# Kernel optimization log

Hardware: AMD Instinct MI355X
Metric: run time of the kernel (lower is better)

Reference implementation:

```python
import jax, jax.numpy as jnp
import numpy as np
from jax import lax

B, T_ENC, T_DEC, H = 512, 64, 18, 128
NF = 17  # input_size - 1 (column 14 is dropped)
COLS = np.array(list(range(14)) + list(range(15, 18)))


def _lstm_cell(x, h, c, Wih, Whh, bih, bhh):
    # PyTorch LSTMCell: gates = x@Wih^T + bih + h@Whh^T + bhh, order i,f,g,o
    g = x @ Wih.T + bih + h @ Whh.T + bhh
    i, f, gg, o = jnp.split(g, 4, axis=-1)
    c2 = jax.nn.sigmoid(f) * c + jax.nn.sigmoid(i) * jnp.tanh(gg)
    h2 = jax.nn.sigmoid(o) * jnp.tanh(c2)
    return h2, c2


def setup_inputs() -> dict:
    key = jax.random.key(0)
    ks = jax.random.split(key, 32)
    s = 0.08
    def w(k, shape):
        return jax.random.normal(k, shape, jnp.float32) * s
    return {
        "input_p_q": jax.random.normal(ks[0], (B, T_ENC, 18), jnp.float32),
        "label_p": jax.random.normal(ks[1], (B, T_ENC), jnp.float32),
        "Wih1": w(ks[2], (4 * H, NF)), "Whh1": w(ks[3], (4 * H, H)),
        "bih1": w(ks[4], (4 * H,)), "bhh1": w(ks[5], (4 * H,)),
        "Wih2": w(ks[6], (4 * H, H + 1)), "Whh2": w(ks[7], (4 * H, H)),
        "bih2": w(ks[8], (4 * H,)), "bhh2": w(ks[9], (4 * H,)),
        "Wihd": w(ks[10], (4 * H, H)), "Whhd": w(ks[11], (4 * H, H)),
        "bihd": w(ks[12], (4 * H,)), "bhhd": w(ks[13], (4 * H,)),
        "Wi_w": w(ks[14], (T_ENC, T_ENC)), "Wi_b": w(ks[15], (T_ENC,)),
        "We_w": w(ks[16], (T_ENC, 2 * H)),
        "Vd_w": w(ks[17], (1, T_ENC)), "Vd_b": w(ks[18], (1,)),
        "Wi2_w": w(ks[19], (T_ENC, T_ENC)), "Wi2_b": w(ks[20], (T_ENC,)),
        "We2_w": w(ks[21], (T_ENC, 2 * H)),
        "Vd2_w": w(ks[22], (1, T_ENC)), "Vd2_b": w(ks[23], (1,)),
        "Wx_w": w(ks[24], (H, H)), "Wx_b": w(ks[25], (H,)),
        "Wh_w": w(ks[26], (H, 2 * H)),
        "V_w": w(ks[27], (1, H)), "V_b": w(ks[28], (1,)),
        "reg_w": w(ks[29], (1, H)), "reg_b": w(ks[30], (1,)),
    }


def reference(input_p_q, label_p, Wih1, Whh1, bih1, bhh1, Wih2, Whh2, bih2, bhh2,
              Wihd, Whhd, bihd, bhhd, Wi_w, Wi_b, We_w, Vd_w, Vd_b,
              Wi2_w, Wi2_b, We2_w, Vd2_w, Vd2_b, Wx_w, Wx_b, Wh_w, V_w, V_b,
              reg_w, reg_b):
    B_ = input_p_q.shape[0]
    inputs = input_p_q[:, :T_ENC, COLS]  # [B, T, 17]
    z = jnp.zeros((B_, H), input_p_q.dtype)

    # stage 1: per-step spatial attention over the 17 driving series + LSTM encoder
    WiX = jnp.swapaxes(inputs, 1, 2) @ Wi_w.T + Wi_b  # [B, 17, T] (step-invariant)
    def step1(carry, x_t):
        h, c = carry
        e = jnp.concatenate([h, c], axis=-1) @ We_w.T  # [B, T]
        score = jnp.tanh(WiX + e[:, None, :]) @ Vd_w[0] + Vd_b[0]  # [B, 17]
        a = jax.nn.softmax(score, axis=1)
        h, c = _lstm_cell(x_t * a, h, c, Wih1, Whh1, bih1, bhh1)
        return (h, c), h
    _, mid = lax.scan(step1, (z, z), jnp.swapaxes(inputs, 0, 1))
    mid = jnp.swapaxes(mid, 0, 1)  # [B, T, H]
    mid2 = jnp.concatenate([mid, label_p[:, :T_ENC, None]], axis=2)  # [B, T, H+1]

    # stage 2: spatial attention over H+1 channels + second LSTM encoder
    Wi2X = jnp.swapaxes(mid2, 1, 2) @ Wi2_w.T + Wi2_b  # [B, H+1, T]
    def step2(carry, x_t):
        h, c = carry
        e = jnp.concatenate([h, c], axis=-1) @ We2_w.T  # [B, T]
        score = jnp.tanh(Wi2X + e[:, None, :]) @ Vd2_w[0] + Vd2_b[0]  # [B, H+1]
        a = jax.nn.softmax(score, axis=1)
        h, c = _lstm_cell(x_t * a, h, c, Wih2, Whh2, bih2, bhh2)
        return (h, c), h
    _, final = lax.scan(step2, (z, z), jnp.swapaxes(mid2, 0, 1))
    final = jnp.swapaxes(final, 0, 1)  # [B, T, H]

    # stage 3: temporal attention decoder for T_DEC + 6 steps
    WxF = final @ Wx_w.T + Wx_b  # [B, T, H] (step-invariant)
    def step3(carry, _):
        h, c = carry
        e = jnp.concatenate([h, c], axis=-1) @ Wh_w.T  # [B, H]
        s = jnp.tanh(WxF + e[:, None, :]) @ V_w[0] + V_b[0]  # [B, T]
        a = jax.nn.softmax(s, axis=1)
        din = jnp.einsum('bt,bth->bh', a, final)  # context vector
        h, c = _lstm_cell(din, h, c, Wihd, Whhd, bihd, bhhd)
        return (h, c), h
    _, dec = lax.scan(step3, (z, z), None, length=T_DEC + 6)
    dec = jnp.swapaxes(dec, 0, 1)  # [B, T_DEC+6, H]
    out = dec @ reg_w[0] + reg_b[0]  # [B, T_DEC+6]
    return out[:, -T_DEC:]
```

## Files before the change

kernel.cpp:

```cpp
#include <hip/hip_runtime.h>
#include <hip/hip_fp16.h>

#define TENC 64
#define TDEC 18
#define NDEC 24
#define NF1  17
#define NF2  129
#define HH   128

#define OFF_WI   0
#define OFF_WI2  4096
#define U_GB   8192
#define U_GDH  45568
#define U_GDX  78336
#define U_GFH  111616
#define U_GFX  144384
#define U_WE   177152
#define U_WE2  185344
#define U_WH   193536
#define U_WXH  209920

#define SB   68
#define SWF  132
#define XIN  1200
#define BIGN 8772

typedef _Float16 h2t __attribute__((ext_vector_type(2)));

#if defined(__has_builtin)
#if __has_builtin(__builtin_amdgcn_fdot2)
#define HAVE_FDOT2 1
#endif
#endif

template<int I> struct ic_t { static constexpr int v = I; };
template<int N, typename F>
__device__ __forceinline__ void sfor(F&& f)
{
    if constexpr (N > 0) { sfor<N - 1>((F&&)f); f(ic_t<N - 1>{}); }
}

__device__ __forceinline__ float fdot2p(unsigned w, unsigned x, float acc)
{
    h2t hw = __builtin_bit_cast(h2t, w);
    h2t hx = __builtin_bit_cast(h2t, x);
#ifdef HAVE_FDOT2
    return __builtin_amdgcn_fdot2(hw, hx, acc, false);
#else
    return acc + (float)hw.x * (float)hx.x + (float)hw.y * (float)hx.y;
#endif
}

__device__ __forceinline__ unsigned pkh_d(float a, float b)
{
    __half ha = __float2half(a), hb = __float2half(b);
    return (unsigned)__half_as_ushort(ha) | ((unsigned)__half_as_ushort(hb) << 16);
}

__device__ __forceinline__ float hget(unsigned u, int hi)
{
    h2t v = __builtin_bit_cast(h2t, u);
    return hi ? (float)v.y : (float)v.x;
}

__device__ __forceinline__ float fsig(float x) { return 1.f / (1.f + __expf(-x)); }
__device__ __forceinline__ float ftanh(float x)
{
    x = fminf(fmaxf(x, -15.f), 15.f);
    float e = __expf(2.f * x);
    return (e - 1.f) / (e + 1.f);
}

__global__ void pack_f2(const float* Wi, const float* Wi2, float* ws)
{
    const int m = blockIdx.y;
    const float* src = m ? Wi2 : Wi;
    const int off = m ? OFF_WI2 : OFF_WI;
    const int G = 64, K = 64, n = G * K;
    for (int i = blockIdx.x * blockDim.x + threadIdx.x; i < n; i += gridDim.x * blockDim.x) {
        int q = i & 3, gk = i >> 2;
        int kk = gk / G, g = gk - kk * G;
        ws[off + i] = src[g * K + kk * 4 + q];
    }
}

__global__ void pack_gp(const float* Wih, const float* Whh, int Kx, int KXP, int qbase,
                        unsigned base, int ldg, unsigned* wsu)
{
    const int g = threadIdx.x;
    const int q = qbase + blockIdx.x;
    int k0 = 2 * q, k1 = 2 * q + 1;
    float f0 = (k0 < KXP) ? ((k0 < Kx) ? Wih[g * Kx + k0] : 0.f) : Whh[g * HH + (k0 - KXP)];
    float f1 = (k1 < KXP) ? ((k1 < Kx) ? Wih[g * Kx + k1] : 0.f) : Whh[g * HH + (k1 - KXP)];
    wsu[base + (unsigned)blockIdx.x * (unsigned)ldg + g] = pkh_d(f0, f1);
}

__global__ void pack_ew(const float* W, int J, int nPQ, int nI, unsigned base, unsigned* wsu)
{
    int idx = blockIdx.x * blockDim.x + threadIdx.x;
    if (idx >= J * 128) return;
    int j = idx >> 7, r = idx & 127;
    int pq = r / nI, i = r - pq * nI;
    int pr = i * nPQ + pq;
    wsu[base + idx] = pkh_d(W[j * 256 + 2 * pr], W[j * 256 + 2 * pr + 1]);
}

__global__ __launch_bounds__(512, 2)
void dstp_main(const float* __restrict__ inq, const float* __restrict__ labp,
               const float* __restrict__ bih1, const float* __restrict__ bhh1,
               const float* __restrict__ bih2, const float* __restrict__ bhh2,
               const float* __restrict__ bihd, const float* __restrict__ bhhd,
               const float* __restrict__ Wi_b, const float* __restrict__ Vd_w, const float* __restrict__ Vd_b,
               const float* __restrict__ Wi2_b, const float* __restrict__ Vd2_w, const float* __restrict__ Vd2_b,
               const float* __restrict__ Wx_b, const float* __restrict__ V_w, const float* __restrict__ V_b,
               const float* __restrict__ reg_w, const float* __restrict__ reg_b,
               const float* __restrict__ ws, float* __restrict__ out)
{
    __shared__ __align__(16) unsigned buf_h[2][TENC][64];
    __shared__ __align__(16) float big[2][BIGN];
    __shared__ __align__(16) unsigned hcp[2][128];
    __shared__ __align__(16) unsigned xhp[2][132];
    __shared__ __align__(16) float ebuf[2][128];
    __shared__ float sc[2][132];
    __shared__ float att[2][64];
    __shared__ float pre[2][512];
    __shared__ float preH[2][512];
    __shared__ float lab[2][64];
    __shared__ __align__(16) float vw1[64], vw2[64], vwf[128], rw[128];
    __shared__ float rsm[4];

    const int tid  = threadIdx.x;
    const int b0   = blockIdx.x * 2;
    const unsigned* wsu = (const unsigned*)ws;
    const float4* Wip  = (const float4*)(ws + OFF_WI);
    const float4* Wi2p = (const float4*)(ws + OFF_WI2);

    const float bg1 = bih1[tid] + bhh1[tid];
    const float bg2 = bih2[tid] + bhh2[tid];
    const float bgd = bihd[tid] + bhhd[tid];
    float creg = 0.f;

    if (tid < 128) lab[tid >> 6][tid & 63] = labp[(b0 + (tid >> 6)) * TENC + (tid & 63)];
    if (tid < 64)        vw1[tid]       = Vd_w[tid];
    else if (tid < 128)  vw2[tid - 64]  = Vd2_w[tid - 64];
    else if (tid < 256)  vwf[tid - 128] = V_w[tid - 128];
    else if (tid < 384)  rw[tid - 256]  = reg_w[tid - 256];
    for (int i = tid; i < 2176; i += 512) {
        int bb = i / 1088, r = i - bb * 1088, t = r / NF1, f = r - t * NF1;
        big[bb][XIN + r] = inq[((b0 + bb) * TENC + t) * 18 + f + (f >= 14)];
    }
    __syncthreads();
    for (int i = tid; i < 2176; i += 512) {
        int bb = i / 1088, r = i - bb * 1088, f = r >> 6, j = r & 63;
        float acc = Wi_b[j];
        for (int tt = 0; tt < 16; ++tt) {
            float4 w = Wip[tt * 64 + j];
            acc += big[bb][XIN + (4 * tt + 0) * NF1 + f] * w.x
                 + big[bb][XIN + (4 * tt + 1) * NF1 + f] * w.y
                 + big[bb][XIN + (4 * tt + 2) * NF1 + f] * w.z
                 + big[bb][XIN + (4 * tt + 3) * NF1 + f] * w.w;
        }
        big[bb][f * SB + j] = acc;
    }

    {
        if (tid < 256) hcp[tid >> 7][tid & 127] = 0u;
        if (tid < 264) xhp[tid / 132][tid % 132] = 0u;
        creg = 0.f;
        unsigned wB[73];
        sfor<73>([&](auto I) { wB[I.v] = wsu[U_GB + I.v * 512 + tid]; });
        unsigned we[16];
        const int ewb = U_WE + ((tid >> 3) << 7) + ((tid & 7) << 4);
        sfor<16>([&](auto I) { we[I.v] = wsu[ewb + I.v]; });
        __syncthreads();

        for (int t = 0; t < TENC; ++t) {
            {
                int j = tid >> 3, pq = tid & 7;
                float a0 = 0.f, a1 = 0.f, b0c = 0.f, b1c = 0.f;
                sfor<8>([&](auto I) {
                    a0  = fdot2p(we[I.v], hcp[0][I.v * 8 + pq], a0);
                    a1  = fdot2p(we[I.v], hcp[1][I.v * 8 + pq], a1);
                    b0c = fdot2p(we[8 + I.v], hcp[0][(8 + I.v) * 8 + pq], b0c);
                    b1c = fdot2p(we[8 + I.v], hcp[1][(8 + I.v) * 8 + pq], b1c);
                });
                float s0 = a0 + b0c, s1 = a1 + b1c;
                s0 += __shfl_xor(s0, 1, 8); s1 += __shfl_xor(s1, 1, 8);
                s0 += __shfl_xor(s0, 2, 8); s1 += __shfl_xor(s1, 2, 8);
                s0 += __shfl_xor(s0, 4, 8); s1 += __shfl_xor(s1, 4, 8);
                if (pq == 0) { ebuf[0][j] = s0; ebuf[1][j] = s1; }
            }
            __syncthreads();
            {
                const uint4* h0q = (const uint4*)hcp[0];
                const uint4* h1q = (const uint4*)hcp[1];
                float q0 = 0.f, q1 = 0.f, q2 = 0.f, q3 = 0.f;
                sfor<16>([&](auto C) {
                    uint4 H0 = h0q[C.v], H1 = h1q[C.v];
                    q0 = fdot2p(wB[9 + 4 * C.v + 0], H0.x, q0);
                    q2 = fdot2p(wB[9 + 4 * C.v + 0], H1.x, q2);
                    q1 = fdot2p(wB[9 + 4 * C.v + 1], H0.y, q1);
                    q3 = fdot2p(wB[9 + 4 * C.v + 1], H1.y, q3);
                    q0 = fdot2p(wB[9 + 4 * C.v + 2], H0.z, q0);
                    q2 = fdot2p(wB[9 + 4 * C.v + 2], H1.z, q2);
                    q1 = fdot2p(wB[9 + 4 * C.v + 3], H0.w, q1);
                    q3 = fdot2p(wB[9 + 4 * C.v + 3], H1.w, q3);
                });
                preH[0][tid] = q0 + q1;
                preH[1][tid] = q2 + q3;
            }
            for (int i = tid; i < 544; i += 512) {
                int bb = i / 272, r = i - bb * 272, f = r >> 4, pp = r & 15;
                float4 wx = *(const float4*)&big[bb][f * SB + pp * 4];
                float4 e4 = *(const float4*)&ebuf[bb][pp * 4];
                float4 v4 = *(const float4*)&vw1[pp * 4];
                float acc = ftanh(wx.x + e4.x) * v4.x + ftanh(wx.y + e4.y) * v4.y
                          + ftanh(wx.z + e4.z) * v4.z + ftanh(wx.w + e4.w) * v4.w;
                acc += __shfl_xor(acc, 1, 16);
                acc += __shfl_xor(acc, 2, 16);
                acc += __shfl_xor(acc, 4, 16);
                acc += __shfl_xor(acc, 8, 16);
                if (pp == 0) sc[bb][f] = acc + Vd_b[0];
            }
            __syncthreads();
            if (tid < 128) {
                int bb = tid >> 6, l = tid & 63;
                float e = (l < NF1) ? __expf(sc[bb][l]) : 0.f;
                float s = e;
                for (int d = 32; d; d >>= 1) s += __shfl_xor(s, d, 64);
                float xv = (l < NF1) ? big[bb][XIN + t * NF1 + l] * (e / s) : 0.f;
                float xp = __shfl_xor(xv, 1, 64);
                if (!(l & 1) && l < 18) xhp[bb][l >> 1] = pkh_d(xv, xp);
            }
            __syncthreads();
            {
                const uint4* x0q = (const uint4*)xhp[0];
                const uint4* x1q = (const uint4*)xhp[1];
                float p00 = bg1, p10 = bg1;
                sfor<2>([&](auto C) {
                    uint4 X0 = x0q[C.v], X1 = x1q[C.v];
                    p00 = fdot2p(wB[4 * C.v + 0], X0.x, p00);
                    p10 = fdot2p(wB[4 * C.v + 0], X1.x, p10);
                    p00 = fdot2p(wB[4 * C.v + 1], X0.y, p00);
                    p10 = fdot2p(wB[4 * C.v + 1], X1.y, p10);
                    p00 = fdot2p(wB[4 * C.v + 2], X0.z, p00);
                    p10 = fdot2p(wB[4 * C.v + 2], X1.z, p10);
                    p00 = fdot2p(wB[4 * C.v + 3], X0.w, p00);
                    p10 = fdot2p(wB[4 * C.v + 3], X1.w, p10);
                });
                p00 = fdot2p(wB[8], xhp[0][8], p00);
                p10 = fdot2p(wB[8], xhp[1][8], p10);
                pre[0][tid] = p00 + preH[0][tid];
                pre[1][tid] = p10 + preH[1][tid];
            }
            __syncthreads();
            if (tid < 256) {
                int bb = tid >> 7, k = tid & 127;
                float gi = pre[bb][k], gf = pre[bb][128 + k], gg = pre[bb][256 + k], go = pre[bb][384 + k];
                float c2 = fsig(gf) * creg + fsig(gi) * ftanh(gg);
                float h2v = fsig(go) * ftanh(c2);
                creg = c2;
                float hp = __shfl_xor(h2v, 1, 64);
                float cp = __shfl_xor(c2, 1, 64);
                if (!(k & 1)) {
                    unsigned hu = pkh_d(h2v, hp);
                    hcp[bb][k >> 1] = hu;
                    hcp[bb][64 + (k >> 1)] = pkh_d(c2, cp);
                    buf_h[bb][t][k >> 1] = hu;
                }
            }
            __syncthreads();
        }
    }

    if (tid < 256) hcp[tid >> 7][tid & 127] = 0u;
    if (tid < 264) xhp[tid / 132][tid % 132] = 0u;
    creg = 0.f;
    for (int i = tid; i < 16512; i += 512) {
        int bb = i / 8256, r = i - bb * 8256, f = r >> 6, j = r & 63;
        float acc = Wi2_b[j];
        if (f < HH) {
            int fp = f >> 1, fh = f & 1;
            for (int tt = 0; tt < 16; ++tt) {
                float4 w = Wi2p[tt * 64 + j];
                acc += hget(buf_h[bb][4 * tt + 0][fp], fh) * w.x
                     + hget(buf_h[bb][4 * tt + 1][fp], fh) * w.y
                     + hget(buf_h[bb][4 * tt + 2][fp], fh) * w.z
                     + hget(buf_h[bb][4 * tt + 3][fp], fh) * w.w;
            }
        } else {
            for (int tt = 0; tt < 16; ++tt) {
                float4 w = Wi2p[tt * 64 + j];
                acc += lab[bb][4 * tt] * w.x + lab[bb][4 * tt + 1] * w.y
                     + lab[bb][4 * tt + 2] * w.z + lab[bb][4 * tt + 3] * w.w;
            }
        }
        big[bb][f * SB + j] = acc;
    }

    {
        unsigned wD[129];
        sfor<65>([&](auto I) { wD[I.v] = wsu[U_GDX + I.v * 512 + tid]; });
        sfor<64>([&](auto I) { wD[65 + I.v] = wsu[U_GDH + I.v * 512 + tid]; });
        unsigned wes[16];
        const int ewb2 = U_WE2 + ((tid >> 3) << 7) + ((tid & 7) << 4);
        sfor<16>([&](auto I) { wes[I.v] = wsu[ewb2 + I.v]; });
        __syncthreads();

        for (int t = 0; t < TENC; ++t) {
            {
                int j = tid >> 3, pq = tid & 7;
                float a0 = 0.f, a1 = 0.f, b0c = 0.f, b1c = 0.f;
                sfor<8>([&](auto I) {
                    a0  = fdot2p(wes[I.v], hcp[0][I.v * 8 + pq], a0);
                    a1  = fdot2p(wes[I.v], hcp[1][I.v * 8 + pq], a1);
                    b0c = fdot2p(wes[8 + I.v], hcp[0][(8 + I.v) * 8 + pq], b0c);
                    b1c = fdot2p(wes[8 + I.v], hcp[1][(8 + I.v) * 8 + pq], b1c);
                });
                float s0 = a0 + b0c, s1 = a1 + b1c;
                s0 += __shfl_xor(s0, 1, 8); s1 += __shfl_xor(s1, 1, 8);
                s0 += __shfl_xor(s0, 2, 8); s1 += __shfl_xor(s1, 2, 8);
                s0 += __shfl_xor(s0, 4, 8); s1 += __shfl_xor(s1, 4, 8);
                if (pq == 0) { ebuf[0][j] = s0; ebuf[1][j] = s1; }
            }
            __syncthreads();
            {
                const uint4* h0q = (const uint4*)hcp[0];
                const uint4* h1q = (const uint4*)hcp[1];
                float q0 = 0.f, q1 = 0.f, q2 = 0.f, q3 = 0.f;
                sfor<16>([&](auto C) {
                    uint4 H0 = h0q[C.v], H1 = h1q[C.v];
                    q0 = fdot2p(wD[65 + 4 * C.v + 0], H0.x, q0);
                    q2 = fdot2p(wD[65 + 4 * C.v + 0], H1.x, q2);
                    q1 = fdot2p(wD[65 + 4 * C.v + 1], H0.y, q1);
                    q3 = fdot2p(wD[65 + 4 * C.v + 1], H1.y, q3);
                    q0 = fdot2p(wD[65 + 4 * C.v + 2], H0.z, q0);
                    q2 = fdot2p(wD[65 + 4 * C.v + 2], H1.z, q2);
                    q1 = fdot2p(wD[65 + 4 * C.v + 3], H0.w, q1);
                    q3 = fdot2p(wD[65 + 4 * C.v + 3], H1.w, q3);
                });
                preH[0][tid] = q0 + q1;
                preH[1][tid] = q2 + q3;
            }
            for (int i = tid; i < 1032; i += 512) {
                int bb = i / 516, r = i - bb * 516, f = r >> 2, pp = r & 3;
                float acc = 0.f;
                #pragma unroll
                for (int c = 0; c < 4; ++c) {
                    float4 wx = *(const float4*)&big[bb][f * SB + pp * 16 + c * 4];
                    float4 e4 = *(const float4*)&ebuf[bb][pp * 16 + c * 4];
                    float4 v4 = *(const float4*)&vw2[pp * 16 + c * 4];
                    acc += ftanh(wx.x + e4.x) * v4.x + ftanh(wx.y + e4.y) * v4.y
                         + ftanh(wx.z + e4.z) * v4.z + ftanh(wx.w + e4.w) * v4.w;
                }
                acc += __shfl_xor(acc, 1, 4);
                acc += __shfl_xor(acc, 2, 4);
                if (pp == 0) sc[bb][f] = acc + Vd2_b[0];
            }
            __syncthreads();
            if (tid < 128) {
                int bb = tid >> 6, l = tid & 63;
                float e1 = __expf(sc[bb][l]);
                float e2 = __expf(sc[bb][l + 64]);
                float e3 = (l == 0) ? __expf(sc[bb][128]) : 0.f;
                float s = e1 + e2 + e3;
                for (int d = 32; d; d >>= 1) s += __shfl_xor(s, d, 64);
                float inv = 1.f / s;
                float v1 = hget(buf_h[bb][t][l >> 1], l & 1) * e1 * inv;
                float v2 = hget(buf_h[bb][t][32 + (l >> 1)], l & 1) * e2 * inv;
                float v1p = __shfl_xor(v1, 1, 64);
                float v2p = __shfl_xor(v2, 1, 64);
                if (!(l & 1)) {
                    xhp[bb][l >> 1] = pkh_d(v1, v1p);
                    xhp[bb][32 + (l >> 1)] = pkh_d(v2, v2p);
                }
                if (l == 0) xhp[bb][64] = pkh_d(lab[bb][t] * e3 * inv, 0.f);
            }
            __syncthreads();
            {
                const uint4* x0q = (const uint4*)xhp[0];
                const uint4* x1q = (const uint4*)xhp[1];
                float p00 = bg2, p01 = 0.f, p10 = bg2, p11 = 0.f;
                sfor<16>([&](auto C) {
                    uint4 X0 = x0q[C.v], X1 = x1q[C.v];
                    p00 = fdot2p(wD[4 * C.v + 0], X0.x, p00);
                    p10 = fdot2p(wD[4 * C.v + 0], X1.x, p10);
                    p01 = fdot2p(wD[4 * C.v + 1], X0.y, p01);
                    p11 = fdot2p(wD[4 * C.v + 1], X1.y, p11);
                    p00 = fdot2p(wD[4 * C.v + 2], X0.z, p00);
                    p10 = fdot2p(wD[4 * C.v + 2], X1.z, p10);
                    p01 = fdot2p(wD[4 * C.v + 3], X0.w, p01);
                    p11 = fdot2p(wD[4 * C.v + 3], X1.w, p11);
                });
                p00 = fdot2p(wD[64], xhp[0][64], p00);
                p10 = fdot2p(wD[64], xhp[1][64], p10);
                pre[0][tid] = (p00 + p01) + preH[0][tid];
                pre[1][tid] = (p10 + p11) + preH[1][tid];
            }
            __syncthreads();
            if (tid < 256) {
                int bb = tid >> 7, k = tid & 127;
                float gi = pre[bb][k], gf = pre[bb][128 + k], gg = pre[bb][256 + k], go = pre[bb][384 + k];
                float c2 = fsig(gf) * creg + fsig(gi) * ftanh(gg);
                float h2v = fsig(go) * ftanh(c2);
                creg = c2;
                float hp = __shfl_xor(h2v, 1, 64);
                float cp = __shfl_xor(c2, 1, 64);
                if (!(k & 1)) {
                    unsigned hu = pkh_d(h2v, hp);
                    hcp[bb][k >> 1] = hu;
                    hcp[bb][64 + (k >> 1)] = pkh_d(c2, cp);
                    buf_h[bb][t][k >> 1] = hu;
                }
            }
            __syncthreads();
        }
    }

    if (tid < 256) hcp[tid >> 7][tid & 127] = 0u;
    if (tid < 264) xhp[tid / 132][tid % 132] = 0u;
    creg = 0.f;
    {
        const int j = tid & 127;
        unsigned wxh[64];
        sfor<64>([&](auto I) { wxh[I.v] = wsu[U_WXH + I.v * 128 + j]; });
        for (int u = tid >> 7; u < 128; u += 4) {
            int bb = u >> 6, tt = u & 63;
            const uint4* bq = (const uint4*)buf_h[bb][tt];
            float a0 = Wx_b[j], a1 = 0.f, a2 = 0.f, a3 = 0.f;
            sfor<16>([&](auto C) {
                uint4 X = bq[C.v];
                a0 = fdot2p(wxh[4 * C.v + 0], X.x, a0);
                a1 = fdot2p(wxh[4 * C.v + 1], X.y, a1);
                a2 = fdot2p(wxh[4 * C.v + 2], X.z, a2);
                a3 = fdot2p(wxh[4 * C.v + 3], X.w, a3);
            });
            big[bb][tt * SWF + j] = (a0 + a1) + (a2 + a3);
        }
    }

    {
        unsigned wF[128];
        sfor<64>([&](auto I) { wF[I.v] = wsu[U_GFX + I.v * 512 + tid]; });
        sfor<64>([&](auto I) { wF[64 + I.v] = wsu[U_GFH + I.v * 512 + tid]; });
        unsigned wh[32];
        const int whb = U_WH + ((tid >> 2) << 7) + ((tid & 3) << 5);
        sfor<32>([&](auto I) { wh[I.v] = wsu[whb + I.v]; });
        __syncthreads();

        for (int n = 0; n < NDEC; ++n) {
            {
                int j = tid >> 2, pq = tid & 3;
                float a0 = 0.f, a1 = 0.f, b0c = 0.f, b1c = 0.f;
                sfor<16>([&](auto I) {
                    a0  = fdot2p(wh[I.v], hcp[0][I.v * 4 + pq], a0);
                    a1  = fdot2p(wh[I.v], hcp[1][I.v * 4 + pq], a1);
                    b0c = fdot2p(wh[16 + I.v], hcp[0][(16 + I.v) * 4 + pq], b0c);
                    b1c = fdot2p(wh[16 + I.v], hcp[1][(16 + I.v) * 4 + pq], b1c);
                });
                float s0 = a0 + b0c, s1 = a1 + b1c;
                s0 += __shfl_xor(s0, 1, 4); s1 += __shfl_xor(s1, 1, 4);
                s0 += __shfl_xor(s0, 2, 4); s1 += __shfl_xor(s1, 2, 4);
                if (pq == 0) { ebuf[0][j] = s0; ebuf[1][j] = s1; }
            }
            __syncthreads();
            {
                const uint4* h0q = (const uint4*)hcp[0];
                const uint4* h1q = (const uint4*)hcp[1];
                float q0 = 0.f, q1 = 0.f, q2 = 0.f, q3 = 0.f;
                sfor<16>([&](auto C) {
                    uint4 H0 = h0q[C.v], H1 = h1q[C.v];
                    q0 = fdot2p(wF[64 + 4 * C.v + 0], H0.x, q0);
                    q2 = fdot2p(wF[64 + 4 * C.v + 0], H1.x, q2);
                    q1 = fdot2p(wF[64 + 4 * C.v + 1], H0.y, q1);
                    q3 = fdot2p(wF[64 + 4 * C.v + 1], H1.y, q3);
                    q0 = fdot2p(wF[64 + 4 * C.v + 2], H0.z, q0);
                    q2 = fdot2p(wF[64 + 4 * C.v + 2], H1.z, q2);
                    q1 = fdot2p(wF[64 + 4 * C.v + 3], H0.w, q1);
                    q3 = fdot2p(wF[64 + 4 * C.v + 3], H1.w, q3);
                });
                preH[0][tid] = q0 + q1;
                preH[1][tid] = q2 + q3;
            }
            for (int i = tid; i < 1024; i += 512) {
                int bb = i >> 9, r = i & 511, tt = r >> 3, pp = r & 7;
                float acc = 0.f;
                #pragma unroll
                for (int c = 0; c < 4; ++c) {
                    float4 wx = *(const float4*)&big[bb][tt * SWF + pp * 16 + c * 4];
                    float4 e4 = *(const float4*)&ebuf[bb][pp * 16 + c * 4];
                    float4 v4 = *(const float4*)&vwf[pp * 16 + c * 4];
                    acc += ftanh(wx.x + e4.x) * v4.x + ftanh(wx.y + e4.y) * v4.y
                         + ftanh(wx.z + e4.z) * v4.z + ftanh(wx.w + e4.w) * v4.w;
                }
                acc += __shfl_xor(acc, 1, 8);
                acc += __shfl_xor(acc, 2, 8);
                acc += __shfl_xor(acc, 4, 8);
                if (pp == 0) sc[bb][tt] = acc + V_b[0];
            }
            __syncthreads();
            if (tid < 128) {
                int bb = tid >> 6, l = tid & 63;
                float e = __expf(sc[bb][l]);
                float s = e;
                for (int d = 32; d; d >>= 1) s += __shfl_xor(s, d, 64);
                att[bb][l] = e / s;
            }
            __syncthreads();
            for (int i = tid; i < 1024; i += 512) {
                int bb = i >> 9, r = i & 511, k = r >> 2, pq = r & 3;
                int kp = k >> 1, kh = k & 1;
                float acc = 0.f;
                #pragma unroll
                for (int u = 0; u < 16; ++u) {
                    int tt = u * 4 + pq;
                    acc += att[bb][tt] * hget(buf_h[bb][tt][kp], kh);
                }
                acc += __shfl_xor(acc, 1, 64);
                acc += __shfl_xor(acc, 2, 64);
                float dp = __shfl_xor(acc, 4, 64);
                if ((r & 7) == 0) xhp[bb][r >> 3] = pkh_d(acc, dp);
            }
            __syncthreads();
            {
                const uint4* x0q = (const uint4*)xhp[0];
                const uint4* x1q = (const uint4*)xhp[1];
                float p00 = bgd, p01 = 0.f, p10 = bgd, p11 = 0.f;
                sfor<16>([&](auto C) {
                    uint4 X0 = x0q[C.v], X1 = x1q[C.v];
                    p00 = fdot2p(wF[4 * C.v + 0], X0.x, p00);
                    p10 = fdot2p(wF[4 * C.v + 0], X1.x, p10);
                    p01 = fdot2p(wF[4 * C.v + 1], X0.y, p01);
                    p11 = fdot2p(wF[4 * C.v + 1], X1.y, p11);
                    p00 = fdot2p(wF[4 * C.v + 2], X0.z, p00);
                    p10 = fdot2p(wF[4 * C.v + 2], X1.z, p10);
                    p01 = fdot2p(wF[4 * C.v + 3], X0.w, p01);
                    p11 = fdot2p(wF[4 * C.v + 3], X1.w, p11);
                });
                pre[0][tid] = (p00 + p01) + preH[0][tid];
                pre[1][tid] = (p10 + p11) + preH[1][tid];
            }
            __syncthreads();
            if (tid < 256) {
                int bb = tid >> 7, k = tid & 127;
                float gi = pre[bb][k], gf = pre[bb][128 + k], gg = pre[bb][256 + k], go = pre[bb][384 + k];
                float c2 = fsig(gf) * creg + fsig(gi) * ftanh(gg);
                float h2v = fsig(go) * ftanh(c2);
                creg = c2;
                float hp = __shfl_xor(h2v, 1, 64);
                float cp = __shfl_xor(c2, 1, 64);
                if (!(k & 1)) {
                    unsigned hu = pkh_d(h2v, hp);
                    hcp[bb][k >> 1] = hu;
                    hcp[bb][64 + (k >> 1)] = pkh_d(c2, cp);
                }
                if (n >= 6) {
                    float v = h2v * rw[k];
                    for (int d = 32; d; d >>= 1) v += __shfl_xor(v, d, 64);
                    if ((tid & 63) == 0) rsm[tid >> 6] = v;
                }
            }
            __syncthreads();
            if (n >= 6 && tid < 2)
                out[(b0 + tid) * TDEC + (n - 6)] = rsm[tid * 2] + rsm[tid * 2 + 1] + reg_b[0];
        }
    }
}

extern "C" void kernel_launch(void* const* d_in, const int* in_sizes, int n_in,
                              void* d_out, int out_size, void* d_ws, size_t ws_size,
                              hipStream_t stream)
{
    const float* inq   = (const float*)d_in[0];
    const float* labp  = (const float*)d_in[1];
    const float* Wih1  = (const float*)d_in[2];
    const float* Whh1  = (const float*)d_in[3];
    const float* bih1  = (const float*)d_in[4];
    const float* bhh1  = (const float*)d_in[5];
    const float* Wih2  = (const float*)d_in[6];
    const float* Whh2  = (const float*)d_in[7];
    const float* bih2  = (const float*)d_in[8];
    const float* bhh2  = (const float*)d_in[9];
    const float* Wihd  = (const float*)d_in[10];
    const float* Whhd  = (const float*)d_in[11];
    const float* bihd  = (const float*)d_in[12];
    const float* bhhd  = (const float*)d_in[13];
    const float* Wi_w  = (const float*)d_in[14];
    const float* Wi_b  = (const float*)d_in[15];
    const float* We_w  = (const float*)d_in[16];
    const float* Vd_w  = (const float*)d_in[17];
    const float* Vd_b  = (const float*)d_in[18];
    const float* Wi2_w = (const float*)d_in[19];
    const float* Wi2_b = (const float*)d_in[20];
    const float* We2_w = (const float*)d_in[21];
    const float* Vd2_w = (const float*)d_in[22];
    const float* Vd2_b = (const float*)d_in[23];
    const float* Wx_w  = (const float*)d_in[24];
    const float* Wx_b  = (const float*)d_in[25];
    const float* Wh_w  = (const float*)d_in[26];
    const float* V_w   = (const float*)d_in[27];
    const float* V_b   = (const float*)d_in[28];
    const float* reg_w = (const float*)d_in[29];
    const float* reg_b = (const float*)d_in[30];
    float* ws  = (float*)d_ws;
    unsigned* wsu = (unsigned*)d_ws;
    float* out = (float*)d_out;

    pack_f2<<<dim3(16, 2), 256, 0, stream>>>(Wi_w, Wi2_w, ws);
    pack_gp<<<73, 512, 0, stream>>>(Wih1, Whh1, 17, 18, 0, U_GB, 512, wsu);
    pack_gp<<<65, 512, 0, stream>>>(Wih2, Whh2, 129, 130, 0, U_GDX, 512, wsu);
    pack_gp<<<64, 512, 0, stream>>>(Wih2, Whh2, 129, 130, 65, U_GDH, 512, wsu);
    pack_gp<<<64, 512, 0, stream>>>(Wihd, Whhd, 128, 128, 0, U_GFX, 512, wsu);
    pack_gp<<<64, 512, 0, stream>>>(Wihd, Whhd, 128, 128, 64, U_GFH, 512, wsu);
    pack_gp<<<64, 128, 0, stream>>>(Wx_w, Wx_w, 128, 128, 0, U_WXH, 128, wsu);
    pack_ew<<<8, 1024, 0, stream>>>(We_w, 64, 8, 16, U_WE, wsu);
    pack_ew<<<8, 1024, 0, stream>>>(We2_w, 64, 8, 16, U_WE2, wsu);
    pack_ew<<<16, 1024, 0, stream>>>(Wh_w, 128, 4, 32, U_WH, wsu);
    dstp_main<<<256, 512, 0, stream>>>(inq, labp, bih1, bhh1, bih2, bhh2, bihd, bhhd,
                                       Wi_b, Vd_w, Vd_b, Wi2_b, Vd2_w, Vd2_b,
                                       Wx_b, V_w, V_b, reg_w, reg_b, ws, out);
}
```

Before: 798.9 us.

## Fuse attention score, exp and weighting into one phase with deferred softmax normalization

In all three recurrent stages, the score computation, the exponentiation and the input weighting are merged into a single phase. The softmax denominator is computed through per-wave partial sums in shared memory and applied after the gate matvec (or after the context reduction), not before. This removes one or two block-wide barriers per timestep, on a latency-bound serial recurrence. In exchange, unnormalized exp-weighted inputs are packed to half precision, which risks overflow or precision loss. Lanes with padded feature indices now do some redundant work.

```diff
diff --git a/kernel.cpp b/kernel.cpp
--- a/kernel.cpp
+++ b/kernel.cpp
@@ -121,8 +121,8 @@
     __shared__ __align__(16) unsigned hcp[2][128];
     __shared__ __align__(16) unsigned xhp[2][132];
     __shared__ __align__(16) float ebuf[2][128];
-    __shared__ float sc[2][132];
     __shared__ float att[2][64];
+    __shared__ float ssum[8][2];
     __shared__ float pre[2][512];
     __shared__ float preH[2][512];
     __shared__ float lab[2][64];
@@ -208,35 +208,58 @@
                 });
                 preH[0][tid] = q0 + q1;
                 preH[1][tid] = q2 + q3;
-            }
-            for (int i = tid; i < 544; i += 512) {
-                int bb = i / 272, r = i - bb * 272, f = r >> 4, pp = r & 15;
-                float4 wx = *(const float4*)&big[bb][f * SB + pp * 4];
-                float4 e4 = *(const float4*)&ebuf[bb][pp * 4];
-                float4 v4 = *(const float4*)&vw1[pp * 4];
-                float acc = ftanh(wx.x + e4.x) * v4.x + ftanh(wx.y + e4.y) * v4.y
-                          + ftanh(wx.z + e4.z) * v4.z + ftanh(wx.w + e4.w) * v4.w;
-                acc += __shfl_xor(acc, 1, 16);
-                acc += __shfl_xor(acc, 2, 16);
-                acc += __shfl_xor(acc, 4, 16);
-                acc += __shfl_xor(acc, 8, 16);
-                if (pp == 0) sc[bb][f] = acc + Vd_b[0];
-            }
-            __syncthreads();
-            if (tid < 128) {
-                int bb = tid >> 6, l = tid & 63;
-                float e = (l < NF1) ? __expf(sc[bb][l]) : 0.f;
-                float s = e;
-                for (int d = 32; d; d >>= 1) s += __shfl_xor(s, d, 64);
-                float xv = (l < NF1) ? big[bb][XIN + t * NF1 + l] * (e / s) : 0.f;
-                float xp = __shfl_xor(xv, 1, 64);
-                if (!(l & 1) && l < 18) xhp[bb][l >> 1] = pkh_d(xv, xp);
-            }
-            __syncthreads();
-            {
+
+                float ew0 = 0.f, ew1 = 0.f;
+                {
+                    int i = tid, bb = i / 288, r = i - bb * 288, f = r >> 4, pp = r & 15;
+                    int fc = (f < NF1) ? f : 16;
+                    float4 wx = *(const float4*)&big[bb][fc * SB + pp * 4];
+                    float4 e4 = *(const float4*)&ebuf[bb][pp * 4];
+                    float4 v4 = *(const float4*)&vw1[pp * 4];
+                    float acc = ftanh(wx.x + e4.x) * v4.x + ftanh(wx.y + e4.y) * v4.y
+                              + ftanh(wx.z + e4.z) * v4.z + ftanh(wx.w + e4.w) * v4.w;
+                    acc += __shfl_xor(acc, 1, 16);
+                    acc += __shfl_xor(acc, 2, 16);
+                    acc += __shfl_xor(acc, 4, 16);
+                    acc += __shfl_xor(acc, 8, 16);
+                    float e = (pp == 0 && f < NF1) ? __expf(acc + Vd_b[0]) : 0.f;
+                    float xval = (f < NF1) ? big[bb][XIN + t * NF1 + fc] : 0.f;
+                    float prod = xval * e;
+                    float podd = __shfl_xor(prod, 16, 64);
+                    if ((r & 31) == 0) xhp[bb][f >> 1] = pkh_d(prod, podd);
+                    ew0 += (bb == 0) ? e : 0.f;
+                    ew1 += (bb == 1) ? e : 0.f;
+                }
+                if (tid < 64) {
+                    int i = 512 + tid, bb = 1, r = i - 288, f = r >> 4, pp = r & 15;
+                    int fc = (f < NF1) ? f : 16;
+                    float4 wx = *(const float4*)&big[bb][fc * SB + pp * 4];
+                    float4 e4 = *(const float4*)&ebuf[bb][pp * 4];
+                    float4 v4 = *(const float4*)&vw1[pp * 4];
+                    float acc = ftanh(wx.x + e4.x) * v4.x + ftanh(wx.y + e4.y) * v4.y
+                              + ftanh(wx.z + e4.z) * v4.z + ftanh(wx.w + e4.w) * v4.w;
+                    acc += __shfl_xor(acc, 1, 16);
+                    acc += __shfl_xor(acc, 2, 16);
+                    acc += __shfl_xor(acc, 4, 16);
+                    acc += __shfl_xor(acc, 8, 16);
+                    float e = (pp == 0 && f < NF1) ? __expf(acc + Vd_b[0]) : 0.f;
+                    float xval = (f < NF1) ? big[bb][XIN + t * NF1 + fc] : 0.f;
+                    float prod = xval * e;
+                    float podd = __shfl_xor(prod, 16, 64);
+                    if ((r & 31) == 0) xhp[bb][f >> 1] = pkh_d(prod, podd);
+                    ew1 += e;
+                }
+                for (int d = 32; d; d >>= 1) { ew0 += __shfl_xor(ew0, d, 64); ew1 += __shfl_xor(ew1, d, 64); }
+                if ((tid & 63) == 0) { ssum[tid >> 6][0] = ew0; ssum[tid >> 6][1] = ew1; }
+            }
+            __syncthreads();
+            {
+                float S0 = 0.f, S1 = 0.f;
+                sfor<8>([&](auto W) { S0 += ssum[W.v][0]; S1 += ssum[W.v][1]; });
+                float inv0 = 1.f / S0, inv1 = 1.f / S1;
                 const uint4* x0q = (const uint4*)xhp[0];
                 const uint4* x1q = (const uint4*)xhp[1];
-                float p00 = bg1, p10 = bg1;
+                float p00 = 0.f, p10 = 0.f;
                 sfor<2>([&](auto C) {
                     uint4 X0 = x0q[C.v], X1 = x1q[C.v];
                     p00 = fdot2p(wB[4 * C.v + 0], X0.x, p00);
@@ -250,8 +273,8 @@
                 });
                 p00 = fdot2p(wB[8], xhp[0][8], p00);
                 p10 = fdot2p(wB[8], xhp[1][8], p10);
-                pre[0][tid] = p00 + preH[0][tid];
-                pre[1][tid] = p10 + preH[1][tid];
+                pre[0][tid] = p00 * inv0 + bg1 + preH[0][tid];
+                pre[1][tid] = p10 * inv1 + bg1 + preH[1][tid];
             }
             __syncthreads();
             if (tid < 256) {
@@ -341,46 +364,65 @@
                 });
                 preH[0][tid] = q0 + q1;
                 preH[1][tid] = q2 + q3;
-            }
-            for (int i = tid; i < 1032; i += 512) {
-                int bb = i / 516, r = i - bb * 516, f = r >> 2, pp = r & 3;
-                float acc = 0.f;
+
+                float ew0 = 0.f, ew1 = 0.f;
                 #pragma unroll
-                for (int c = 0; c < 4; ++c) {
-                    float4 wx = *(const float4*)&big[bb][f * SB + pp * 16 + c * 4];
-                    float4 e4 = *(const float4*)&ebuf[bb][pp * 16 + c * 4];
-                    float4 v4 = *(const float4*)&vw2[pp * 16 + c * 4];
-                    acc += ftanh(wx.x + e4.x) * v4.x + ftanh(wx.y + e4.y) * v4.y
-                         + ftanh(wx.z + e4.z) * v4.z + ftanh(wx.w + e4.w) * v4.w;
-                }
-                acc += __shfl_xor(acc, 1, 4);
-                acc += __shfl_xor(acc, 2, 4);
-                if (pp == 0) sc[bb][f] = acc + Vd2_b[0];
-            }
-            __syncthreads();
-            if (tid < 128) {
-                int bb = tid >> 6, l = tid & 63;
-                float e1 = __expf(sc[bb][l]);
-                float e2 = __expf(sc[bb][l + 64]);
-                float e3 = (l == 0) ? __expf(sc[bb][128]) : 0.f;
-                float s = e1 + e2 + e3;
-                for (int d = 32; d; d >>= 1) s += __shfl_xor(s, d, 64);
-                float inv = 1.f / s;
-                float v1 = hget(buf_h[bb][t][l >> 1], l & 1) * e1 * inv;
-                float v2 = hget(buf_h[bb][t][32 + (l >> 1)], l & 1) * e2 * inv;
-                float v1p = __shfl_xor(v1, 1, 64);
-                float v2p = __shfl_xor(v2, 1, 64);
-                if (!(l & 1)) {
-                    xhp[bb][l >> 1] = pkh_d(v1, v1p);
-                    xhp[bb][32 + (l >> 1)] = pkh_d(v2, v2p);
-                }
-                if (l == 0) xhp[bb][64] = pkh_d(lab[bb][t] * e3 * inv, 0.f);
-            }
-            __syncthreads();
-            {
+                for (int it = 0; it < 2; ++it) {
+                    int i = tid + it * 512;
+                    int bb = i / 520, r = i - bb * 520, f = r >> 2, pp = r & 3;
+                    int fc = (f < NF2) ? f : 128;
+                    float acc = 0.f;
+                    #pragma unroll
+                    for (int c = 0; c < 4; ++c) {
+                        float4 wx = *(const float4*)&big[bb][fc * SB + pp * 16 + c * 4];
+                        float4 e4 = *(const float4*)&ebuf[bb][pp * 16 + c * 4];
+                        float4 v4 = *(const float4*)&vw2[pp * 16 + c * 4];
+                        acc += ftanh(wx.x + e4.x) * v4.x + ftanh(wx.y + e4.y) * v4.y
+                             + ftanh(wx.z + e4.z) * v4.z + ftanh(wx.w + e4.w) * v4.w;
+                    }
+                    acc += __shfl_xor(acc, 1, 4);
+                    acc += __shfl_xor(acc, 2, 4);
+                    float e = (pp == 0 && f < NF2) ? __expf(acc + Vd2_b[0]) : 0.f;
+                    float xval = (f < HH) ? hget(buf_h[bb][t][fc >> 1], f & 1) : lab[bb][t];
+                    float prod = xval * e;
+                    float podd = __shfl_xor(prod, 4, 64);
+                    if ((r & 7) == 0) xhp[bb][f >> 1] = pkh_d(prod, podd);
+                    ew0 += (bb == 0) ? e : 0.f;
+                    ew1 += (bb == 1) ? e : 0.f;
+                }
+                if (tid < 16) {
+                    int i = 1024 + tid;
+                    int bb = 1, r = i - 520, f = r >> 2, pp = r & 3;
+                    int fc = (f < NF2) ? f : 128;
+                    float acc = 0.f;
+                    #pragma unroll
+                    for (int c = 0; c < 4; ++c) {
+                        float4 wx = *(const float4*)&big[bb][fc * SB + pp * 16 + c * 4];
+                        float4 e4 = *(const float4*)&ebuf[bb][pp * 16 + c * 4];
+                        float4 v4 = *(const float4*)&vw2[pp * 16 + c * 4];
+                        acc += ftanh(wx.x + e4.x) * v4.x + ftanh(wx.y + e4.y) * v4.y
+                             + ftanh(wx.z + e4.z) * v4.z + ftanh(wx.w + e4.w) * v4.w;
+                    }
+                    acc += __shfl_xor(acc, 1, 4);
+                    acc += __shfl_xor(acc, 2, 4);
+                    float e = (pp == 0 && f < NF2) ? __expf(acc + Vd2_b[0]) : 0.f;
+                    float xval = (f < HH) ? hget(buf_h[bb][t][fc >> 1], f & 1) : lab[bb][t];
+                    float prod = xval * e;
+                    float podd = __shfl_xor(prod, 4, 64);
+                    if ((r & 7) == 0) xhp[bb][f >> 1] = pkh_d(prod, podd);
+                    ew1 += e;
+                }
+                for (int d = 32; d; d >>= 1) { ew0 += __shfl_xor(ew0, d, 64); ew1 += __shfl_xor(ew1, d, 64); }
+                if ((tid & 63) == 0) { ssum[tid >> 6][0] = ew0; ssum[tid >> 6][1] = ew1; }
+            }
+            __syncthreads();
+            {
+                float S0 = 0.f, S1 = 0.f;
+                sfor<8>([&](auto W) { S0 += ssum[W.v][0]; S1 += ssum[W.v][1]; });
+                float inv0 = 1.f / S0, inv1 = 1.f / S1;
                 const uint4* x0q = (const uint4*)xhp[0];
                 const uint4* x1q = (const uint4*)xhp[1];
-                float p00 = bg2, p01 = 0.f, p10 = bg2, p11 = 0.f;
+                float p00 = 0.f, p01 = 0.f, p10 = 0.f, p11 = 0.f;
                 sfor<16>([&](auto C) {
                     uint4 X0 = x0q[C.v], X1 = x1q[C.v];
                     p00 = fdot2p(wD[4 * C.v + 0], X0.x, p00);
@@ -394,8 +436,8 @@
                 });
                 p00 = fdot2p(wD[64], xhp[0][64], p00);
                 p10 = fdot2p(wD[64], xhp[1][64], p10);
-                pre[0][tid] = (p00 + p01) + preH[0][tid];
-                pre[1][tid] = (p10 + p11) + preH[1][tid];
+                pre[0][tid] = (p00 + p01) * inv0 + bg2 + preH[0][tid];
+                pre[1][tid] = (p10 + p11) * inv1 + bg2 + preH[1][tid];
             }
             __syncthreads();
             if (tid < 256) {
@@ -481,45 +523,50 @@
                 });
                 preH[0][tid] = q0 + q1;
                 preH[1][tid] = q2 + q3;
-            }
-            for (int i = tid; i < 1024; i += 512) {
-                int bb = i >> 9, r = i & 511, tt = r >> 3, pp = r & 7;
-                float acc = 0.f;
+
+                float ew0 = 0.f, ew1 = 0.f;
                 #pragma unroll
-                for (int c = 0; c < 4; ++c) {
-                    float4 wx = *(const float4*)&big[bb][tt * SWF + pp * 16 + c * 4];
-                    float4 e4 = *(const float4*)&ebuf[bb][pp * 16 + c * 4];
-                    float4 v4 = *(const float4*)&vwf[pp * 16 + c * 4];
-                    acc += ftanh(wx.x + e4.x) * v4.x + ftanh(wx.y + e4.y) * v4.y
-                         + ftanh(wx.z + e4.z) * v4.z + ftanh(wx.w + e4.w) * v4.w;
-                }
-                acc += __shfl_xor(acc, 1, 8);
-                acc += __shfl_xor(acc, 2, 8);
-                acc += __shfl_xor(acc, 4, 8);
-                if (pp == 0) sc[bb][tt] = acc + V_b[0];
-            }
-            __syncthreads();
-            if (tid < 128) {
-                int bb = tid >> 6, l = tid & 63;
-                float e = __expf(sc[bb][l]);
-                float s = e;
-                for (int d = 32; d; d >>= 1) s += __shfl_xor(s, d, 64);
-                att[bb][l] = e / s;
-            }
-            __syncthreads();
-            for (int i = tid; i < 1024; i += 512) {
-                int bb = i >> 9, r = i & 511, k = r >> 2, pq = r & 3;
-                int kp = k >> 1, kh = k & 1;
-                float acc = 0.f;
-                #pragma unroll
-                for (int u = 0; u < 16; ++u) {
-                    int tt = u * 4 + pq;
-                    acc += att[bb][tt] * hget(buf_h[bb][tt][kp], kh);
-                }
-                acc += __shfl_xor(acc, 1, 64);
-                acc += __shfl_xor(acc, 2, 64);
-                float dp = __shfl_xor(acc, 4, 64);
-                if ((r & 7) == 0) xhp[bb][r >> 3] = pkh_d(acc, dp);
+                for (int it = 0; it < 2; ++it) {
+                    int bb = it, tt = tid >> 3, pp = tid & 7;
+                    float acc = 0.f;
+                    #pragma unroll
+                    for (int c = 0; c < 4; ++c) {
+                        float4 wx = *(const float4*)&big[bb][tt * SWF + pp * 16 + c * 4];
+                        float4 e4 = *(const float4*)&ebuf[bb][pp * 16 + c * 4];
+                        float4 v4 = *(const float4*)&vwf[pp * 16 + c * 4];
+                        acc += ftanh(wx.x + e4.x) * v4.x + ftanh(wx.y + e4.y) * v4.y
+                             + ftanh(wx.z + e4.z) * v4.z + ftanh(wx.w + e4.w) * v4.w;
+                    }
+                    acc += __shfl_xor(acc, 1, 8);
+                    acc += __shfl_xor(acc, 2, 8);
+                    acc += __shfl_xor(acc, 4, 8);
+                    float e = (pp == 0) ? __expf(acc + V_b[0]) : 0.f;
+                    if (pp == 0) att[bb][tt] = e;
+                    if (it == 0) ew0 += e; else ew1 += e;
+                }
+                for (int d = 32; d; d >>= 1) { ew0 += __shfl_xor(ew0, d, 64); ew1 += __shfl_xor(ew1, d, 64); }
+                if ((tid & 63) == 0) { ssum[tid >> 6][0] = ew0; ssum[tid >> 6][1] = ew1; }
+            }
+            __syncthreads();
+            {
+                float S0 = 0.f, S1 = 0.f;
+                sfor<8>([&](auto W) { S0 += ssum[W.v][0]; S1 += ssum[W.v][1]; });
+                float inv0 = 1.f / S0, inv1 = 1.f / S1;
+                for (int i = tid; i < 1024; i += 512) {
+                    int bb = i >> 9, r = i & 511, k = r >> 2, pq = r & 3;
+                    int kp = k >> 1, kh = k & 1;
+                    float acc = 0.f;
+                    #pragma unroll
+                    for (int u = 0; u < 16; ++u) {
+                        int tt = u * 4 + pq;
+                        acc += att[bb][tt] * hget(buf_h[bb][tt][kp], kh);
+                    }
+                    acc += __shfl_xor(acc, 1, 64);
+                    acc += __shfl_xor(acc, 2, 64);
+                    acc *= bb ? inv1 : inv0;
+                    float dp = __shfl_xor(acc, 4, 64);
+                    if ((r & 7) == 0) xhp[bb][r >> 3] = pkh_d(acc, dp);
+                }
             }
             __syncthreads();
             {
```

After: 803.5 us. About the same (+0.6%).

## Permute gate rows so LSTM cell update uses wave shuffles instead of shared barrier

Applied to the files above, without the earlier changes.

Gate weight rows are packed in a permuted order so the four gates (i,f,g,o) of each hidden unit land in four adjacent lanes. The cell update then gathers them with lane shuffles right after the gate dot product. This removes the shared-memory pre-activation buffer and one __syncthreads per recurrent step in all three stages. All 512 threads now do the nonlinearities redundantly in groups of four, and the regression output reduction is spread across 8 waves, which adds some shuffle and ALU work per step.

```diff
diff --git a/kernel.cpp b/kernel.cpp
--- a/kernel.cpp
+++ b/kernel.cpp
@@ -71,6 +71,9 @@
     return (e - 1.f) / (e + 1.f);
 }
 
+__device__ __host__ __forceinline__ int gperm(int tid)
+{ return (tid & 3) * 128 + 16 * (tid >> 6) + ((tid >> 2) & 15); }
+
 __global__ void pack_f2(const float* Wi, const float* Wi2, float* ws)
 {
     const int m = blockIdx.y;
@@ -88,10 +91,11 @@
                         unsigned base, int ldg, unsigned* wsu)
 {
     const int g = threadIdx.x;
+    const int rr = (ldg == 512) ? gperm(g) : g;
     const int q = qbase + blockIdx.x;
     int k0 = 2 * q, k1 = 2 * q + 1;
-    float f0 = (k0 < KXP) ? ((k0 < Kx) ? Wih[g * Kx + k0] : 0.f) : Whh[g * HH + (k0 - KXP)];
-    float f1 = (k1 < KXP) ? ((k1 < Kx) ? Wih[g * Kx + k1] : 0.f) : Whh[g * HH + (k1 - KXP)];
+    float f0 = (k0 < KXP) ? ((k0 < Kx) ? Wih[rr * Kx + k0] : 0.f) : Whh[rr * HH + (k0 - KXP)];
+    float f1 = (k1 < KXP) ? ((k1 < Kx) ? Wih[rr * Kx + k1] : 0.f) : Whh[rr * HH + (k1 - KXP)];
     wsu[base + (unsigned)blockIdx.x * (unsigned)ldg + g] = pkh_d(f0, f1);
 }
 
@@ -123,22 +127,23 @@
     __shared__ __align__(16) float ebuf[2][128];
     __shared__ float sc[2][132];
     __shared__ float att[2][64];
-    __shared__ float pre[2][512];
     __shared__ float preH[2][512];
     __shared__ float lab[2][64];
     __shared__ __align__(16) float vw1[64], vw2[64], vwf[128], rw[128];
-    __shared__ float rsm[4];
+    __shared__ float rsm[8][2];
 
     const int tid  = threadIdx.x;
     const int b0   = blockIdx.x * 2;
+    const int chan = 16 * (tid >> 6) + ((tid >> 2) & 15);
+    const int rr   = gperm(tid);
     const unsigned* wsu = (const unsigned*)ws;
     const float4* Wip  = (const float4*)(ws + OFF_WI);
     const float4* Wi2p = (const float4*)(ws + OFF_WI2);
 
-    const float bg1 = bih1[tid] + bhh1[tid];
-    const float bg2 = bih2[tid] + bhh2[tid];
-    const float bgd = bihd[tid] + bhhd[tid];
-    float creg = 0.f;
+    const float bg1 = bih1[rr] + bhh1[rr];
+    const float bg2 = bih2[rr] + bhh2[rr];
+    const float bgd = bihd[rr] + bhhd[rr];
+    float creg0 = 0.f, creg1 = 0.f;
 
     if (tid < 128) lab[tid >> 6][tid & 63] = labp[(b0 + (tid >> 6)) * TENC + (tid & 63)];
     if (tid < 64)        vw1[tid]       = Vd_w[tid];
@@ -166,7 +171,7 @@
     {
         if (tid < 256) hcp[tid >> 7][tid & 127] = 0u;
         if (tid < 264) xhp[tid / 132][tid % 132] = 0u;
-        creg = 0.f;
+        creg0 = 0.f; creg1 = 0.f;
         unsigned wB[73];
         sfor<73>([&](auto I) { wB[I.v] = wsu[U_GB + I.v * 512 + tid]; });
         unsigned we[16];
@@ -250,23 +255,25 @@
                 });
                 p00 = fdot2p(wB[8], xhp[0][8], p00);
                 p10 = fdot2p(wB[8], xhp[1][8], p10);
-                pre[0][tid] = p00 + preH[0][tid];
-                pre[1][tid] = p10 + preH[1][tid];
-            }
-            __syncthreads();
-            if (tid < 256) {
-                int bb = tid >> 7, k = tid & 127;
-                float gi = pre[bb][k], gf = pre[bb][128 + k], gg = pre[bb][256 + k], go = pre[bb][384 + k];
-                float c2 = fsig(gf) * creg + fsig(gi) * ftanh(gg);
-                float h2v = fsig(go) * ftanh(c2);
-                creg = c2;
-                float hp = __shfl_xor(h2v, 1, 64);
-                float cp = __shfl_xor(c2, 1, 64);
-                if (!(k & 1)) {
-                    unsigned hu = pkh_d(h2v, hp);
-                    hcp[bb][k >> 1] = hu;
-                    hcp[bb][64 + (k >> 1)] = pkh_d(c2, cp);
-                    buf_h[bb][t][k >> 1] = hu;
+                p00 += preH[0][tid];
+                p10 += preH[1][tid];
+                int lb = (tid & 63) & ~3;
+                float gi0 = __shfl(p00, lb, 64),     gf0 = __shfl(p00, lb | 1, 64);
+                float gg0 = __shfl(p00, lb | 2, 64), go0 = __shfl(p00, lb | 3, 64);
+                float gi1 = __shfl(p10, lb, 64),     gf1 = __shfl(p10, lb | 1, 64);
+                float gg1 = __shfl(p10, lb | 2, 64), go1 = __shfl(p10, lb | 3, 64);
+                float c20 = fsig(gf0) * creg0 + fsig(gi0) * ftanh(gg0);
+                float h20 = fsig(go0) * ftanh(c20);  creg0 = c20;
+                float c21 = fsig(gf1) * creg1 + fsig(gi1) * ftanh(gg1);
+                float h21 = fsig(go1) * ftanh(c21);  creg1 = c21;
+                int l4 = ((tid & 63) + 4) & 63;
+                float h20p = __shfl(h20, l4, 64), c20p = __shfl(c20, l4, 64);
+                float h21p = __shfl(h21, l4, 64), c21p = __shfl(c21, l4, 64);
+                if (((tid & 63) & 7) == 0) {
+                    int cp = chan >> 1;
+                    unsigned hu0 = pkh_d(h20, h20p), hu1 = pkh_d(h21, h21p);
+                    hcp[0][cp] = hu0; hcp[0][64 + cp] = pkh_d(c20, c20p); buf_h[0][t][cp] = hu0;
+                    hcp[1][cp] = hu1; hcp[1][64 + cp] = pkh_d(c21, c21p); buf_h[1][t][cp] = hu1;
                 }
             }
             __syncthreads();
@@ -275,7 +282,7 @@
 
     if (tid < 256) hcp[tid >> 7][tid & 127] = 0u;
     if (tid < 264) xhp[tid / 132][tid % 132] = 0u;
-    creg = 0.f;
+    creg0 = 0.f; creg1 = 0.f;
     for (int i = tid; i < 16512; i += 512) {
         int bb = i / 8256, r = i - bb * 8256, f = r >> 6, j = r & 63;
         float acc = Wi2_b[j];
@@ -394,23 +401,25 @@
                 });
                 p00 = fdot2p(wD[64], xhp[0][64], p00);
                 p10 = fdot2p(wD[64], xhp[1][64], p10);
-                pre[0][tid] = (p00 + p01) + preH[0][tid];
-                pre[1][tid] = (p10 + p11) + preH[1][tid];
-            }
-            __syncthreads();
-            if (tid < 256) {
-                int bb = tid >> 7, k = tid & 127;
-                float gi = pre[bb][k], gf = pre[bb][128 + k], gg = pre[bb][256 + k], go = pre[bb][384 + k];
-                float c2 = fsig(gf) * creg + fsig(gi) * ftanh(gg);
-                float h2v = fsig(go) * ftanh(c2);
-                creg = c2;
-                float hp = __shfl_xor(h2v, 1, 64);
-                float cp = __shfl_xor(c2, 1, 64);
-                if (!(k & 1)) {
-                    unsigned hu = pkh_d(h2v, hp);
-                    hcp[bb][k >> 1] = hu;
-                    hcp[bb][64 + (k >> 1)] = pkh_d(c2, cp);
-                    buf_h[bb][t][k >> 1] = hu;
+                float pa = (p00 + p01) + preH[0][tid];
+                float pb = (p10 + p11) + preH[1][tid];
+                int lb = (tid & 63) & ~3;
+                float gi0 = __shfl(pa, lb, 64),     gf0 = __shfl(pa, lb | 1, 64);
+                float gg0 = __shfl(pa, lb | 2, 64), go0 = __shfl(pa, lb | 3, 64);
+                float gi1 = __shfl(pb, lb, 64),     gf1 = __shfl(pb, lb | 1, 64);
+                float gg1 = __shfl(pb, lb | 2, 64), go1 = __shfl(pb, lb | 3, 64);
+                float c20 = fsig(gf0) * creg0 + fsig(gi0) * ftanh(gg0);
+                float h20 = fsig(go0) * ftanh(c20);  creg0 = c20;
+                float c21 = fsig(gf1) * creg1 + fsig(gi1) * ftanh(gg1);
+                float h21 = fsig(go1) * ftanh(c21);  creg1 = c21;
+                int l4 = ((tid & 63) + 4) & 63;
+                float h20p = __shfl(h20, l4, 64), c20p = __shfl(c20, l4, 64);
+                float h21p = __shfl(h21, l4, 64), c21p = __shfl(c21, l4, 64);
+                if (((tid & 63) & 7) == 0) {
+                    int cp = chan >> 1;
+                    unsigned hu0 = pkh_d(h20, h20p), hu1 = pkh_d(h21, h21p);
+                    hcp[0][cp] = hu0; hcp[0][64 + cp] = pkh_d(c20, c20p); buf_h[0][t][cp] = hu0;
+                    hcp[1][cp] = hu1; hcp[1][64 + cp] = pkh_d(c21, c21p); buf_h[1][t][cp] = hu1;
                 }
             }
             __syncthreads();
@@ -419,7 +428,7 @@
 
     if (tid < 256) hcp[tid >> 7][tid & 127] = 0u;
     if (tid < 264) xhp[tid / 132][tid % 132] = 0u;
-    creg = 0.f;
+    creg0 = 0.f; creg1 = 0.f;
     {
         const int j = tid & 127;
         unsigned wxh[64];
@@ -537,32 +546,39 @@
                     p01 = fdot2p(wF[4 * C.v + 3], X0.w, p01);
                     p11 = fdot2p(wF[4 * C.v + 3], X1.w, p11);
                 });
-                pre[0][tid] = (p00 + p01) + preH[0][tid];
-                pre[1][tid] = (p10 + p11) + preH[1][tid];
-            }
-            __syncthreads();
-            if (tid < 256) {
-                int bb = tid >> 7, k = tid & 127;
-                float gi = pre[bb][k], gf = pre[bb][128 + k], gg = pre[bb][256 + k], go = pre[bb][384 + k];
-                float c2 = fsig(gf) * creg + fsig(gi) * ftanh(gg);
-                float h2v = fsig(go) * ftanh(c2);
-                creg = c2;
-                float hp = __shfl_xor(h2v, 1, 64);
-                float cp = __shfl_xor(c2, 1, 64);
-                if (!(k & 1)) {
-                    unsigned hu = pkh_d(h2v, hp);
-                    hcp[bb][k >> 1] = hu;
-                    hcp[bb][64 + (k >> 1)] = pkh_d(c2, cp);
+                float pa = (p00 + p01) + preH[0][tid];
+                float pb = (p10 + p11) + preH[1][tid];
+                int lb = (tid & 63) & ~3;
+                float gi0 = __shfl(pa, lb, 64),     gf0 = __shfl(pa, lb | 1, 64);
+                float gg0 = __shfl(pa, lb | 2, 64), go0 = __shfl(pa, lb | 3, 64);
+                float gi1 = __shfl(pb, lb, 64),     gf1 = __shfl(pb, lb | 1, 64);
+                float gg1 = __shfl(pb, lb | 2, 64), go1 = __shfl(pb, lb | 3, 64);
+                float c20 = fsig(gf0) * creg0 + fsig(gi0) * ftanh(gg0);
+                float h20 = fsig(go0) * ftanh(c20);  creg0 = c20;
+                float c21 = fsig(gf1) * creg1 + fsig(gi1) * ftanh(gg1);
+                float h21 = fsig(go1) * ftanh(c21);  creg1 = c21;
+                int l4 = ((tid & 63) + 4) & 63;
+                float h20p = __shfl(h20, l4, 64), c20p = __shfl(c20, l4, 64);
+                float h21p = __shfl(h21, l4, 64), c21p = __shfl(c21, l4, 64);
+                if (((tid & 63) & 7) == 0) {
+                    int cp = chan >> 1;
+                    unsigned hu0 = pkh_d(h20, h20p), hu1 = pkh_d(h21, h21p);
+                    hcp[0][cp] = hu0; hcp[0][64 + cp] = pkh_d(c20, c20p);
+                    hcp[1][cp] = hu1; hcp[1][64 + cp] = pkh_d(c21, c21p);
                 }
                 if (n >= 6) {
-                    float v = h2v * rw[k];
-                    for (int d = 32; d; d >>= 1) v += __shfl_xor(v, d, 64);
-                    if ((tid & 63) == 0) rsm[tid >> 6] = v;
-                }
-            }
-            __syncthreads();
-            if (n >= 6 && tid < 2)
-                out[(b0 + tid) * TDEC + (n - 6)] = rsm[tid * 2] + rsm[tid * 2 + 1] + reg_b[0];
+                    float v0 = ((tid & 3) == 0) ? h20 * rw[chan] : 0.f;
+                    float v1 = ((tid & 3) == 0) ? h21 * rw[chan] : 0.f;
+                    for (int d = 32; d; d >>= 1) { v0 += __shfl_xor(v0, d, 64); v1 += __shfl_xor(v1, d, 64); }
+                    if ((tid & 63) == 0) { rsm[tid >> 6][0] = v0; rsm[tid >> 6][1] = v1; }
+                }
+            }
+            __syncthreads();
+            if (n >= 6 && tid < 2) {
+                float s = reg_b[0];
+                sfor<8>([&](auto W) { s += rsm[W.v][tid]; });
+                out[(b0 + tid) * TDEC + (n - 6)] = s;
+            }
         }
     }
 }
```

After: 871.1 us. 1.09x slower.
